# Performance work log

Measured on AMD Instinct MI355X. Metric: run time of the kernel, lower is better.

Reference implementation:

```python
import jax, jax.numpy as jnp
import numpy as np

VX, VY = 0.2, 0.2
X_OFF = VX / 2 + 0.0          # vx/2 + pc_range[0]
Y_OFF = VY / 2 + (-40.0)      # vy/2 + pc_range[1]
K = 8                          # hardcoded in GCNLayer
BN_EPS = 1e-3
LRELU_SLOPE = 0.2
V, T, C_IN, C_OUT = 4096, 100, 4, 64


def _gcn_layer(x, conv_w, bn_gamma, bn_beta, bn_mean, bn_var):
    """DGCNN EdgeConv layer. x: [N, T, C]. Returns [N, T, O]."""
    N, Tn, C = x.shape
    # KNN on negative squared distance (self included in topk, as in torch code)
    xx = jnp.sum(x * x, axis=-1)                       # [N, T]
    inner = jnp.einsum('ntc,nsc->nts', x, x)           # [N, T, T]
    neg_dist = 2.0 * inner - xx[:, :, None] - xx[:, None, :]
    _, idx = jax.lax.top_k(neg_dist, K)                # [N, T, K]
    # gather neighbor features: nbr[n,t,k,c] = x[n, idx[n,t,k], c]
    nbr = x[jnp.arange(N)[:, None, None], idx]         # [N, T, K, C]
    xc = x[:, :, None, :]                              # [N, T, 1, C]
    edge = jnp.concatenate(
        [nbr - xc, jnp.broadcast_to(xc, (N, Tn, K, C))], axis=-1)  # [N,T,K,2C]
    # 1x1 conv (no bias) + eval-mode BatchNorm + LeakyReLU(0.2)
    h = jnp.einsum('ntkc,oc->ntko', edge, conv_w)      # [N, T, K, O]
    scale = bn_gamma / jnp.sqrt(bn_var + BN_EPS)
    h = (h - bn_mean) * scale + bn_beta
    h = jax.nn.leaky_relu(h, LRELU_SLOPE)
    return jnp.max(h, axis=2)                          # max over k -> [N, T, O]


def setup_inputs() -> dict:
    key = jax.random.key(0)
    k1, k2, k3, k4, k5, k6 = jax.random.split(key, 6)
    features = jax.random.normal(k1, (V, T, C_IN), dtype=jnp.float32)
    num_voxels = jnp.maximum(
        jax.random.randint(k2, (V,), 0, T), 1).astype(jnp.int32)
    coors = jax.random.randint(k3, (V, 4), 0, 352).astype(jnp.int32)
    # GCNLayer params: Conv2d(18, 64, 1, bias=False) + BatchNorm2d(64)
    conv_w = jax.random.normal(k4, (C_OUT, 18), dtype=jnp.float32) * 0.1
    bn_gamma = jnp.ones((C_OUT,), jnp.float32)
    bn_beta = jnp.zeros((C_OUT,), jnp.float32)
    bn_mean = jax.random.normal(k5, (C_OUT,), jnp.float32) * 0.1
    bn_var = 1.0 + 0.1 * jax.random.uniform(k6, (C_OUT,), jnp.float32)
    return {"features": features, "conv_w": conv_w, "bn_gamma": bn_gamma,
            "bn_beta": bn_beta, "bn_mean": bn_mean, "bn_var": bn_var,
            "num_voxels": num_voxels, "coors": coors}


def reference(features, conv_w, bn_gamma, bn_beta, bn_mean, bn_var,
              num_voxels, coors):
    nv = num_voxels.astype(features.dtype)
    # decorate: cluster offsets (xyz - mean) and pillar-center offsets (xy)
    points_mean = jnp.sum(features[:, :, :3], axis=1, keepdims=True) / nv[:, None, None]
    f_cluster = features[:, :, :3] - points_mean                      # [V,T,3]
    fx = features[:, :, 0] - (coors[:, 3].astype(features.dtype)[:, None] * VX + X_OFF)
    fy = features[:, :, 1] - (coors[:, 2].astype(features.dtype)[:, None] * VY + Y_OFF)
    f_center = jnp.stack([fx, fy], axis=-1)                           # [V,T,2]
    feat = jnp.concatenate([features, f_cluster, f_center], axis=-1)  # [V,T,9]
    # padding mask: point t valid iff t < num_voxels[v]
    mask = (jnp.arange(T)[None, :] < num_voxels[:, None]).astype(features.dtype)
    feat = feat * mask[:, :, None]
    # single GCN (last) layer; batch_process chunking is a no-op mathematically
    out = _gcn_layer(feat, conv_w, bn_gamma, bn_beta, bn_mean, bn_var)  # [V,T,64]
    out = out * mask[:, :, None]            # (+ zeros prev_features_out)
    out = jnp.max(out, axis=1)              # max over points -> [V, 64]
    return out
```

## Files before the change

kernel.cpp:

```cpp
#include <hip/hip_runtime.h>

#define TPTS 100
#define CO   64
#define KK   8

__device__ __forceinline__ unsigned umin_(unsigned a, unsigned b) { return a < b ? a : b; }
__device__ __forceinline__ unsigned umax_(unsigned a, unsigned b) { return a > b ? a : b; }

__device__ __forceinline__ unsigned dist_key(const float4 qt, const float4 qs, unsigned s) {
    float dx = qt.x - qs.x, dy = qt.y - qs.y;
    float dz = qt.z - qs.z, dw = qt.w - qs.w;
    float e = __fmaf_rn(dx, dx, __fmaf_rn(dy, dy, __fmaf_rn(dz, dz, dw * dw)));
    return (__float_as_uint(e) & 0xFFFFFF80u) | s;
}

__global__ __launch_bounds__(256) void dgcnn_kernel(
    const float* __restrict__ features,
    const float* __restrict__ conv_w,
    const float* __restrict__ bn_gamma,
    const float* __restrict__ bn_beta,
    const float* __restrict__ bn_mean,
    const float* __restrict__ bn_var,
    const int*  __restrict__ num_voxels,
    const int*  __restrict__ coors,
    float* __restrict__ out)
{
    __shared__ float s_feat[TPTS][12];
    __shared__ float s_xx[TPTS];
    __shared__ int   s_idx[KK][TPTS];
    __shared__ float s_red[4][CO];
    __shared__ float s_mean[4];
    __shared__ union {
        float stage[TPTS][4];
        float g[TPTS][CO];
    } s_u;

    const float INF = __builtin_inff();
    const int v   = blockIdx.x;
    const int tid = threadIdx.x;
    const int nv  = num_voxels[v];

    float4 f = make_float4(0.f, 0.f, 0.f, 0.f);
    if (tid < TPTS) {
        f = reinterpret_cast<const float4*>(features)[v * TPTS + tid];
        *reinterpret_cast<float4*>(&s_u.stage[tid][0]) = f;
    }
    __syncthreads();

    if (tid < 96) {
        int ch = tid >> 5, j = tid & 31;
        float p = s_u.stage[j][ch] + s_u.stage[j + 32][ch] + s_u.stage[j + 64][ch];
        if (j < 4) p += s_u.stage[j + 96][ch];
        #pragma unroll
        for (int off = 16; off >= 1; off >>= 1)
            p += __shfl_xor(p, off, 32);
        if (j == 0) s_mean[ch] = p / (float)nv;
    }
    __syncthreads();

    if (tid < TPTS) {
        float mask = (tid < nv) ? 1.0f : 0.0f;
        float c3 = (float)coors[v * 4 + 3];
        float c2 = (float)coors[v * 4 + 2];
        float r0 = f.x * mask, r1 = f.y * mask, r2 = f.z * mask, r3 = f.w * mask;
        float r4 = (f.x - s_mean[0]) * mask;
        float r5 = (f.y - s_mean[1]) * mask;
        float r6 = (f.z - s_mean[2]) * mask;
        float r7 = (f.x - (c3 * 0.2f + 0.1f)) * mask;
        float r8 = (f.y - (c2 * 0.2f - 39.9f)) * mask;
        float xx = r0*r0 + r1*r1 + r2*r2 + r3*r3 + r4*r4
                 + r5*r5 + r6*r6 + r7*r7 + r8*r8;
        float4* rowv = reinterpret_cast<float4*>(&s_feat[tid][0]);
        rowv[0] = make_float4(1.7320508075688772f * r0,
                              1.7320508075688772f * r1,
                              1.4142135623730951f * r2, r3);
        rowv[1] = make_float4(r4, r5, r6, r7);
        rowv[2] = make_float4(r8, 0.f, 0.f, 0.f);
        s_xx[tid] = xx;
    }
    __syncthreads();

    const int o = tid & 63;
    const int w = tid >> 6;
    const float sgn = (bn_gamma[o] < 0.f) ? -1.f : 1.f;
    float w2[9];

    if (tid < 128) {
        const int t = tid;
        if (t < nv) {
            const float4 qt = *reinterpret_cast<const float4*>(&s_feat[t][0]);
            unsigned va[KK], vb[KK];
            #pragma unroll
            for (int k = 0; k < KK; ++k) { va[k] = 0xFFFFFFFFu; vb[k] = 0xFFFFFFFFu; }
            int s = 0;
            for (; s + 1 < nv; s += 2) {
                const float4 qa = *reinterpret_cast<const float4*>(&s_feat[s][0]);
                const float4 qb = *reinterpret_cast<const float4*>(&s_feat[s + 1][0]);
                unsigned ka = dist_key(qt, qa, (unsigned)s);
                unsigned kb = dist_key(qt, qb, (unsigned)(s + 1));
                #pragma unroll
                for (int k = 0; k < KK; ++k) {
                    unsigned la = umin_(va[k], ka); ka = umax_(va[k], ka); va[k] = la;
                    unsigned lb = umin_(vb[k], kb); kb = umax_(vb[k], kb); vb[k] = lb;
                }
            }
            if (s < nv) {
                const float4 qa = *reinterpret_cast<const float4*>(&s_feat[s][0]);
                unsigned ka = dist_key(qt, qa, (unsigned)s);
                #pragma unroll
                for (int k = 0; k < KK; ++k) {
                    unsigned la = umin_(va[k], ka); ka = umax_(va[k], ka); va[k] = la;
                }
            }
            {
                int mcnt = TPTS - nv; if (mcnt > KK) mcnt = KK;
                unsigned kmb = __float_as_uint(s_xx[t]) & 0xFFFFFF80u;
                for (int j = 0; j < mcnt; ++j) {
                    unsigned km = kmb | (unsigned)(nv + j);
                    if (j & 1) {
                        #pragma unroll
                        for (int k = 0; k < KK; ++k) {
                            unsigned lb = umin_(vb[k], km); km = umax_(vb[k], km); vb[k] = lb;
                        }
                    } else {
                        #pragma unroll
                        for (int k = 0; k < KK; ++k) {
                            unsigned la = umin_(va[k], km); km = umax_(va[k], km); va[k] = la;
                        }
                    }
                }
            }
            #pragma unroll
            for (int k = 0; k < KK; ++k) {
                unsigned key = umin_(va[k], vb[KK - 1 - k]);
                s_idx[k][t] = (int)(key & 127u);
            }
        }
        #pragma unroll
        for (int c = 0; c < 9; ++c) {
            const float ws = (c == 0 || c == 1) ? 0.57735026918962576f
                           : (c == 2) ? 0.70710678118654752f : 1.f;
            float a = conv_w[o * 18 + c];
            float b = conv_w[o * 18 + 9 + c];
            w2[c] = (b - a) * sgn * ws;
        }
    } else {
        float w1[9];
        #pragma unroll
        for (int c = 0; c < 9; ++c) {
            const float ws = (c == 0 || c == 1) ? 0.57735026918962576f
                           : (c == 2) ? 0.70710678118654752f : 1.f;
            float a = conv_w[o * 18 + c];
            float b = conv_w[o * 18 + 9 + c];
            w1[c] = a * sgn * ws;
            w2[c] = (b - a) * sgn * ws;
        }
        const int half = w - 2;
        for (int j = 0; j < 50; ++j) {
            int sR = half * 50 + j;
            const float4* row = reinterpret_cast<const float4*>(&s_feat[sR][0]);
            float4 a = row[0], b = row[1];
            float c8 = s_feat[sR][8];
            float g = a.x * w1[0];
            g = __fmaf_rn(a.y, w1[1], g);
            g = __fmaf_rn(a.z, w1[2], g);
            g = __fmaf_rn(a.w, w1[3], g);
            g = __fmaf_rn(b.x, w1[4], g);
            g = __fmaf_rn(b.y, w1[5], g);
            g = __fmaf_rn(b.z, w1[6], g);
            g = __fmaf_rn(b.w, w1[7], g);
            g = __fmaf_rn(c8,  w1[8], g);
            s_u.g[sR][o] = g;
        }
    }
    __syncthreads();

    float acc = -INF;
    for (int t = w; t < nv; t += 4) {
        const float4* row = reinterpret_cast<const float4*>(&s_feat[t][0]);
        float4 a = row[0], b = row[1];
        float c8 = s_feat[t][8];
        float base = a.x * w2[0];
        base = __fmaf_rn(a.y, w2[1], base);
        base = __fmaf_rn(a.z, w2[2], base);
        base = __fmaf_rn(a.w, w2[3], base);
        base = __fmaf_rn(b.x, w2[4], base);
        base = __fmaf_rn(b.y, w2[5], base);
        base = __fmaf_rn(b.z, w2[6], base);
        base = __fmaf_rn(b.w, w2[7], base);
        base = __fmaf_rn(c8,  w2[8], base);
        int i0 = s_idx[0][t], i1 = s_idx[1][t], i2 = s_idx[2][t], i3 = s_idx[3][t];
        int i4 = s_idx[4][t], i5 = s_idx[5][t], i6 = s_idx[6][t], i7 = s_idx[7][t];
        float g0 = s_u.g[i0][o], g1 = s_u.g[i1][o], g2 = s_u.g[i2][o], g3 = s_u.g[i3][o];
        float g4 = s_u.g[i4][o], g5 = s_u.g[i5][o], g6 = s_u.g[i6][o], g7 = s_u.g[i7][o];
        float gm = fmaxf(fmaxf(fmaxf(g0, g1), fmaxf(g2, g3)),
                         fmaxf(fmaxf(g4, g5), fmaxf(g6, g7)));
        acc = fmaxf(acc, gm + base);
    }
    s_red[w][o] = acc;
    __syncthreads();

    if (tid < CO) {
        float m = fmaxf(fmaxf(s_red[0][tid], s_red[1][tid]),
                        fmaxf(s_red[2][tid], s_red[3][tid]));
        float scale = bn_gamma[tid] / sqrtf(bn_var[tid] + 0.001f);
        float bias  = bn_beta[tid] - bn_mean[tid] * scale;
        float h = m * fabsf(scale) + bias;
        float a = (h > 0.f) ? h : 0.2f * h;
        if (nv < TPTS) a = fmaxf(a, 0.f);
        out[v * CO + tid] = a;
    }
}

extern "C" void kernel_launch(void* const* d_in, const int* in_sizes, int n_in,
                              void* d_out, int out_size, void* d_ws, size_t ws_size,
                              hipStream_t stream) {
    const float* features = (const float*)d_in[0];
    const float* conv_w   = (const float*)d_in[1];
    const float* bn_gamma = (const float*)d_in[2];
    const float* bn_beta  = (const float*)d_in[3];
    const float* bn_mean  = (const float*)d_in[4];
    const float* bn_var   = (const float*)d_in[5];
    const int*   num_vox  = (const int*)d_in[6];
    const int*   coor     = (const int*)d_in[7];
    float* outp = (float*)d_out;
    const int V = in_sizes[6];
    dgcnn_kernel<<<V, 256, 0, stream>>>(features, conv_w, bn_gamma, bn_beta,
                                        bn_mean, bn_var, num_vox, coor, outp);
}
```

Measured before the change: 124.1 us.

## Split KNN source range across both thread halves and share gather precompute

The KNN top-8 search for each point is now split across all 256 threads: the lower 128 threads scan the first half of the source points and the upper 128 scan the second half plus the masked padding entries. The two sorted lists are merged through shared memory. The per-row neighbor projection precompute is spread over all four waves instead of two. The aim is to balance the work that previously sat idle in half the block and to shorten the serial KNN scan, at the cost of an extra barrier and a shared-memory merge step.

```diff
diff --git a/kernel.cpp b/kernel.cpp
--- a/kernel.cpp
+++ b/kernel.cpp
@@ -78,108 +78,93 @@
         rowv[2] = make_float4(r8, 0.f, 0.f, 0.f);
         s_xx[tid] = xx;
     }
-    __syncthreads();
 
     const int o = tid & 63;
     const int w = tid >> 6;
     const float sgn = (bn_gamma[o] < 0.f) ? -1.f : 1.f;
-    float w2[9];
-
-    if (tid < 128) {
-        const int t = tid;
-        if (t < nv) {
-            const float4 qt = *reinterpret_cast<const float4*>(&s_feat[t][0]);
-            unsigned va[KK], vb[KK];
+    float w1[9], w2[9];
+    #pragma unroll
+    for (int c = 0; c < 9; ++c) {
+        const float ws = (c == 0 || c == 1) ? 0.57735026918962576f
+                       : (c == 2) ? 0.70710678118654752f : 1.f;
+        float a = conv_w[o * 18 + c];
+        float b = conv_w[o * 18 + 9 + c];
+        w1[c] = a * sgn * ws;
+        w2[c] = (b - a) * sgn * ws;
+    }
+    __syncthreads();
+
+    const int side = tid >> 7;
+    const int t    = tid & 127;
+    unsigned val[KK];
+    if (t < nv) {
+        const float4 qt = *reinterpret_cast<const float4*>(&s_feat[t][0]);
+        #pragma unroll
+        for (int k = 0; k < KK; ++k) val[k] = 0xFFFFFFFFu;
+        const int h  = (nv + 1) >> 1;
+        const int lo = side ? h : 0;
+        const int hi = side ? nv : h;
+        for (int s = lo; s < hi; ++s) {
+            const float4 qs = *reinterpret_cast<const float4*>(&s_feat[s][0]);
+            unsigned key = dist_key(qt, qs, (unsigned)s);
             #pragma unroll
-            for (int k = 0; k < KK; ++k) { va[k] = 0xFFFFFFFFu; vb[k] = 0xFFFFFFFFu; }
-            int s = 0;
-            for (; s + 1 < nv; s += 2) {
-                const float4 qa = *reinterpret_cast<const float4*>(&s_feat[s][0]);
-                const float4 qb = *reinterpret_cast<const float4*>(&s_feat[s + 1][0]);
-                unsigned ka = dist_key(qt, qa, (unsigned)s);
-                unsigned kb = dist_key(qt, qb, (unsigned)(s + 1));
+            for (int k = 0; k < KK; ++k) {
+                unsigned l = umin_(val[k], key);
+                key = umax_(val[k], key);
+                val[k] = l;
+            }
+        }
+        if (side) {
+            int mcnt = TPTS - nv; if (mcnt > KK) mcnt = KK;
+            unsigned kmb = __float_as_uint(s_xx[t]) & 0xFFFFFF80u;
+            for (int j = 0; j < mcnt; ++j) {
+                unsigned key = kmb | (unsigned)(nv + j);
                 #pragma unroll
                 for (int k = 0; k < KK; ++k) {
-                    unsigned la = umin_(va[k], ka); ka = umax_(va[k], ka); va[k] = la;
-                    unsigned lb = umin_(vb[k], kb); kb = umax_(vb[k], kb); vb[k] = lb;
+                    unsigned l = umin_(val[k], key);
+                    key = umax_(val[k], key);
+                    val[k] = l;
                 }
             }
-            if (s < nv) {
-                const float4 qa = *reinterpret_cast<const float4*>(&s_feat[s][0]);
-                unsigned ka = dist_key(qt, qa, (unsigned)s);
-                #pragma unroll
-                for (int k = 0; k < KK; ++k) {
-                    unsigned la = umin_(va[k], ka); ka = umax_(va[k], ka); va[k] = la;
-                }
-            }
-            {
-                int mcnt = TPTS - nv; if (mcnt > KK) mcnt = KK;
-                unsigned kmb = __float_as_uint(s_xx[t]) & 0xFFFFFF80u;
-                for (int j = 0; j < mcnt; ++j) {
-                    unsigned km = kmb | (unsigned)(nv + j);
-                    if (j & 1) {
-                        #pragma unroll
-                        for (int k = 0; k < KK; ++k) {
-                            unsigned lb = umin_(vb[k], km); km = umax_(vb[k], km); vb[k] = lb;
-                        }
-                    } else {
-                        #pragma unroll
-                        for (int k = 0; k < KK; ++k) {
-                            unsigned la = umin_(va[k], km); km = umax_(va[k], km); va[k] = la;
-                        }
-                    }
-                }
-            }
+        } else {
             #pragma unroll
-            for (int k = 0; k < KK; ++k) {
-                unsigned key = umin_(va[k], vb[KK - 1 - k]);
-                s_idx[k][t] = (int)(key & 127u);
-            }
+            for (int k = 0; k < KK; ++k) s_idx[k][t] = (int)val[k];
         }
-        #pragma unroll
-        for (int c = 0; c < 9; ++c) {
-            const float ws = (c == 0 || c == 1) ? 0.57735026918962576f
-                           : (c == 2) ? 0.70710678118654752f : 1.f;
-            float a = conv_w[o * 18 + c];
-            float b = conv_w[o * 18 + 9 + c];
-            w2[c] = (b - a) * sgn * ws;
-        }
-    } else {
-        float w1[9];
-        #pragma unroll
-        for (int c = 0; c < 9; ++c) {
-            const float ws = (c == 0 || c == 1) ? 0.57735026918962576f
-                           : (c == 2) ? 0.70710678118654752f : 1.f;
-            float a = conv_w[o * 18 + c];
-            float b = conv_w[o * 18 + 9 + c];
-            w1[c] = a * sgn * ws;
-            w2[c] = (b - a) * sgn * ws;
-        }
-        const int half = w - 2;
-        for (int j = 0; j < 50; ++j) {
-            int sR = half * 50 + j;
-            const float4* row = reinterpret_cast<const float4*>(&s_feat[sR][0]);
-            float4 a = row[0], b = row[1];
-            float c8 = s_feat[sR][8];
-            float g = a.x * w1[0];
-            g = __fmaf_rn(a.y, w1[1], g);
-            g = __fmaf_rn(a.z, w1[2], g);
-            g = __fmaf_rn(a.w, w1[3], g);
-            g = __fmaf_rn(b.x, w1[4], g);
-            g = __fmaf_rn(b.y, w1[5], g);
-            g = __fmaf_rn(b.z, w1[6], g);
-            g = __fmaf_rn(b.w, w1[7], g);
-            g = __fmaf_rn(c8,  w1[8], g);
-            s_u.g[sR][o] = g;
-        }
+    }
+    __syncthreads();
+
+    if (side && t < nv) {
+        unsigned a[KK];
+        #pragma unroll
+        for (int k = 0; k < KK; ++k) a[k] = (unsigned)s_idx[k][t];
+        #pragma unroll
+        for (int k = 0; k < KK; ++k)
+            s_idx[k][t] = (int)(umin_(a[k], val[KK - 1 - k]) & 127u);
+    }
+
+    for (int j = 0; j < 25; ++j) {
+        int sR = w * 25 + j;
+        const float4* row = reinterpret_cast<const float4*>(&s_feat[sR][0]);
+        float4 a = row[0], b = row[1];
+        float c8 = s_feat[sR][8];
+        float g = a.x * w1[0];
+        g = __fmaf_rn(a.y, w1[1], g);
+        g = __fmaf_rn(a.z, w1[2], g);
+        g = __fmaf_rn(a.w, w1[3], g);
+        g = __fmaf_rn(b.x, w1[4], g);
+        g = __fmaf_rn(b.y, w1[5], g);
+        g = __fmaf_rn(b.z, w1[6], g);
+        g = __fmaf_rn(b.w, w1[7], g);
+        g = __fmaf_rn(c8,  w1[8], g);
+        s_u.g[sR][o] = g;
     }
     __syncthreads();
 
     float acc = -INF;
-    for (int t = w; t < nv; t += 4) {
-        const float4* row = reinterpret_cast<const float4*>(&s_feat[t][0]);
+    for (int tt = w; tt < nv; tt += 4) {
+        const float4* row = reinterpret_cast<const float4*>(&s_feat[tt][0]);
         float4 a = row[0], b = row[1];
-        float c8 = s_feat[t][8];
+        float c8 = s_feat[tt][8];
         float base = a.x * w2[0];
         base = __fmaf_rn(a.y, w2[1], base);
         base = __fmaf_rn(a.z, w2[2], base);
@@ -189,8 +174,8 @@
         base = __fmaf_rn(b.z, w2[6], base);
         base = __fmaf_rn(b.w, w2[7], base);
         base = __fmaf_rn(c8,  w2[8], base);
-        int i0 = s_idx[0][t], i1 = s_idx[1][t], i2 = s_idx[2][t], i3 = s_idx[3][t];
-        int i4 = s_idx[4][t], i5 = s_idx[5][t], i6 = s_idx[6][t], i7 = s_idx[7][t];
+        int i0 = s_idx[0][tt], i1 = s_idx[1][tt], i2 = s_idx[2][tt], i3 = s_idx[3][tt];
+        int i4 = s_idx[4][tt], i5 = s_idx[5][tt], i6 = s_idx[6][tt], i7 = s_idx[7][tt];
         float g0 = s_u.g[i0][o], g1 = s_u.g[i1][o], g2 = s_u.g[i2][o], g3 = s_u.g[i3][o];
         float g4 = s_u.g[i4][o], g5 = s_u.g[i5][o], g6 = s_u.g[i6][o], g7 = s_u.g[i7][o];
         float gm = fmaxf(fmaxf(fmaxf(g0, g1), fmaxf(g2, g3)),
```

Result: no change. 123.0 us (-0.9%).
